# Kernel optimization log

Hardware: AMD Instinct MI355X
Metric: run time of the kernel (lower is better)

## Reference

```python
import jax, jax.numpy as jnp
import numpy as np


def _mlp(x, W1, b1, W2, b2):
    # x: (B, M, T); torch MLPLayer: transpose(1,2) -> Linear -> Linear -> LeakyReLU -> transpose back
    h = jnp.einsum('bmt,hm->bht', x, W1) + b1[None, :, None]   # (B, H, T)
    y = jnp.einsum('bht,oh->bot', h, W2) + b2[None, :, None]   # (B, M, T)
    return jax.nn.leaky_relu(y, negative_slope=0.01)


def _calc_attn(q, k, v):
    # q: (B, M, Tq), k: (B, M, Tk), v: (B, M, Tk)
    Tq = q.shape[-1]
    qk = jnp.einsum('bmq,bmk->bqk', q, k)                       # (B, Tq, Tk)
    eye = jnp.eye(Tq, dtype=qk.dtype)                           # broadcasts: (Tq,Tq) or (1,1)
    logits = jnp.exp(qk - qk * eye / jnp.sqrt(jnp.asarray(Tq, qk.dtype)))
    scores = jax.nn.softmax(logits, axis=-1)
    return jnp.einsum('bqk,bmk->bmq', scores, v)                # (B, M, Tq)


def setup_inputs() -> dict:
    key = jax.random.key(0)
    B, M, T, H = 16, 128, 2048, 512
    ks = jax.random.split(key, 14)
    s = 0.02
    inp = {
        'pattern': jax.random.normal(ks[0], (B, M, T), jnp.float32),
        'value': jax.random.normal(ks[1], (B, M, T), jnp.float32),
        'kernel_size': 33,
    }
    names = ['q', 'k', 'o']
    for i, n in enumerate(names):
        inp['W%s1' % n] = jax.random.normal(ks[2 + 4 * i], (H, M), jnp.float32) * s
        inp['b%s1' % n] = jax.random.normal(ks[3 + 4 * i], (H,), jnp.float32) * s
        inp['W%s2' % n] = jax.random.normal(ks[4 + 4 * i], (M, H), jnp.float32) * s
        inp['b%s2' % n] = jax.random.normal(ks[5 + 4 * i], (M,), jnp.float32) * s
    return inp


def reference(pattern, value, kernel_size, Wq1, bq1, Wq2, bq2, Wk1, bk1, Wk2, bk2, Wo1, bo1, Wo2, bo2):
    query = _mlp(pattern, Wq1, bq1, Wq2, bq2)
    key = _mlp(pattern, Wk1, bk1, Wk2, bk2)
    # full (internal) attention
    attn_in = _calc_attn(query, key, value)                     # (B, M, T)
    rep_in = _mlp(attn_in, Wo1, bo1, Wo2, bo2)
    # windowed (external) attention
    T = query.shape[-1]
    cu = (kernel_size - 1) // 2
    q_w = query[..., T - 1 - cu : T - cu]                       # (B, M, 1)
    k_w = key[..., kernel_size - cu - 1 : T - cu - 2]           # (B, M, T-k-1)
    v_w = value[..., kernel_size : T - 1]                       # (B, M, T-k-1)
    attn_ex = _calc_attn(q_w, k_w, v_w)                         # (B, M, 1)
    rep_ex = _mlp(attn_ex, Wo1, bo1, Wo2, bo2)
    return jnp.concatenate([rep_in, rep_ex], axis=-1)           # (B, M, T+1)
```

## Files before the change

### kernel.cpp

```cpp
#include <hip/hip_runtime.h>
#include <math.h>

#define B_    16
#define M_    128
#define T_    2048
#define H_    512
#define TOUT_ 2049

typedef unsigned short u16;
typedef unsigned int   u32;
typedef __bf16 bf16x8 __attribute__((ext_vector_type(8)));
typedef float  f32x16 __attribute__((ext_vector_type(16)));
typedef u32    u32x4  __attribute__((ext_vector_type(4)));
typedef u32    u32x2  __attribute__((ext_vector_type(2)));

#define A_OFF     0
#define C_OFF     49152
#define MEAN_OFF  49536
#define AQKBF_OFF 51584
#define AOBF_OFF  67968
#define QT_OFF    76160
#define KT_OFF    (76160 + 2097152)
#define VB_OFF    (76160 + 2 * 2097152)

static __device__ __forceinline__ u16 f2bf(float f) {
  u32 u = __float_as_uint(f);
  u = (u + 0x7FFFu + ((u >> 16) & 1u)) >> 16;
  return (u16)u;
}
static __device__ __forceinline__ u32 pk2(float lo, float hi) {
  return (u32)f2bf(lo) | ((u32)f2bf(hi) << 16);
}
static __device__ __forceinline__ bf16x8 ldfrag(const u16* p) {
  return __builtin_bit_cast(bf16x8, *(const u32x4*)p);
}

__global__ __launch_bounds__(128) void fuse_weights_all(
    const float* __restrict__ W1q, const float* __restrict__ b1q,
    const float* __restrict__ W2q, const float* __restrict__ b2q,
    const float* __restrict__ W1k, const float* __restrict__ b1k,
    const float* __restrict__ W2k, const float* __restrict__ b2k,
    const float* __restrict__ W1o, const float* __restrict__ b1o,
    const float* __restrict__ W2o, const float* __restrict__ b2o,
    float* __restrict__ A, float* __restrict__ c,
    u16* __restrict__ Aqk_bf, u16* __restrict__ Ao_bf) {
  __shared__ float w2row[H_];
  int which = blockIdx.x >> 7;
  int o = blockIdx.x & 127;
  const float* W1 = which == 0 ? W1q : which == 1 ? W1k : W1o;
  const float* b1 = which == 0 ? b1q : which == 1 ? b1k : b1o;
  const float* W2 = which == 0 ? W2q : which == 1 ? W2k : W2o;
  const float* b2 = which == 0 ? b2q : which == 1 ? b2k : b2o;
  int m = threadIdx.x;
  for (int h = m; h < H_; h += 128) w2row[h] = W2[o * H_ + h];
  __syncthreads();
  float acc = 0.f;
  for (int h = 0; h < H_; ++h) acc = fmaf(w2row[h], W1[h * M_ + m], acc);
  A[which * 16384 + o * M_ + m] = acc;
  u16 ab = f2bf(acc);
  if (which == 0)      Aqk_bf[o * 128 + m] = ab;
  else if (which == 1) Aqk_bf[(128 + o) * 128 + m] = ab;
  else                 Ao_bf[o * 128 + m] = ab;
  if (m == 0) {
    float cc = b2[o];
    for (int h = 0; h < H_; ++h) cc = fmaf(w2row[h], b1[h], cc);
    c[which * 128 + o] = cc;
  }
}

#define XSTR 136

__global__ __launch_bounds__(256) void mlp_qk_fused(
    const float* __restrict__ pattern, const u16* __restrict__ Aqk_bf,
    const float* __restrict__ cqk, u16* __restrict__ qT, u16* __restrict__ kT) {
  __shared__ alignas(16) u16 xs[64 * XSTR];
  int b = blockIdx.y;
  int t0 = blockIdx.x * 64;
  int tid = threadIdx.x;
  int lane = tid & 63;
  int wv = tid >> 6;
  int l31 = lane & 31;
  int lh8 = (lane >> 5) * 8;

  bf16x8 afr[2][8];
#pragma unroll
  for (int i = 0; i < 2; ++i) {
    const u16* ap = Aqk_bf + ((2 * wv + i) * 32 + l31) * 128 + lh8;
#pragma unroll
    for (int s = 0; s < 8; ++s) afr[i][s] = ldfrag(ap + 16 * s);
  }

  {
    int mp = tid & 63;
    int tc = tid >> 6;
    const float* r0 = pattern + ((size_t)(b * M_ + 2 * mp)) * T_ + t0 + tc * 16;
    const float* r1 = r0 + T_;
    u32* xw = (u32*)xs;
#pragma unroll
    for (int j = 0; j < 4; ++j) {
      float4 a = *(const float4*)(r0 + 4 * j);
      float4 bb = *(const float4*)(r1 + 4 * j);
      int tt = tc * 16 + 4 * j;
      xw[(tt + 0) * 68 + mp] = pk2(a.x, bb.x);
      xw[(tt + 1) * 68 + mp] = pk2(a.y, bb.y);
      xw[(tt + 2) * 68 + mp] = pk2(a.z, bb.z);
      xw[(tt + 3) * 68 + mp] = pk2(a.w, bb.w);
    }
  }
  __syncthreads();

#pragma unroll
  for (int tt = 0; tt < 2; ++tt) {
    bf16x8 bfr[8];
    const u16* bp = &xs[(tt * 32 + l31) * XSTR + lh8];
#pragma unroll
    for (int s = 0; s < 8; ++s) bfr[s] = ldfrag(bp + 16 * s);
#pragma unroll
    for (int i = 0; i < 2; ++i) {
      f32x16 acc;
#pragma unroll
      for (int r = 0; r < 16; ++r) acc[r] = 0.f;
#pragma unroll
      for (int s = 0; s < 8; ++s)
        acc = __builtin_amdgcn_mfma_f32_32x32x16_bf16(afr[i][s], bfr[s], acc, 0, 0, 0);
      int ot = 2 * wv + i;
      u16* dst = (ot < 4) ? qT : kT;
      int ob = (ot & 3) * 32;
      size_t trow = ((size_t)(b * T_ + t0 + tt * 32 + l31)) * 128;
#pragma unroll
      for (int g = 0; g < 4; ++g) {
        int o0 = 8 * g + 4 * (lane >> 5);
        float v0 = acc[4 * g + 0] + cqk[ot * 32 + o0 + 0];
        float v1 = acc[4 * g + 1] + cqk[ot * 32 + o0 + 1];
        float v2 = acc[4 * g + 2] + cqk[ot * 32 + o0 + 2];
        float v3 = acc[4 * g + 3] + cqk[ot * 32 + o0 + 3];
        v0 = v0 > 0.f ? v0 : 0.01f * v0;
        v1 = v1 > 0.f ? v1 : 0.01f * v1;
        v2 = v2 > 0.f ? v2 : 0.01f * v2;
        v3 = v3 > 0.f ? v3 : 0.01f * v3;
        u32x2 w = {pk2(v0, v1), pk2(v2, v3)};
        *(u32x2*)(dst + trow + ob + o0) = w;
      }
    }
  }
}

__global__ __launch_bounds__(256) void vcast_mean(
    const float* __restrict__ v, u16* __restrict__ vb, float* __restrict__ meanv) {
  __shared__ float red[256];
  int bm = blockIdx.x;
  int tid = threadIdx.x;
  const float* row = v + (size_t)bm * T_;
  int i0 = tid * 8;
  float4 a = *(const float4*)(row + i0);
  float4 bq = *(const float4*)(row + i0 + 4);
  u32x4 o = {pk2(a.x, a.y), pk2(a.z, a.w), pk2(bq.x, bq.y), pk2(bq.z, bq.w)};
  *(u32x4*)&vb[(size_t)bm * T_ + i0] = o;
  float vals[8] = {a.x, a.y, a.z, a.w, bq.x, bq.y, bq.z, bq.w};
  float s = 0.f;
#pragma unroll
  for (int j = 0; j < 8; ++j) {
    int idx = i0 + j;
    if (idx >= 33 && idx < T_ - 1) s += vals[j];
  }
  red[tid] = s;
  __syncthreads();
  for (int st = 128; st > 0; st >>= 1) {
    if (tid < st) red[tid] += red[tid + st];
    __syncthreads();
  }
  if (tid == 0) meanv[bm] = red[0] * (1.f / 2014.f);
}

#define TQ 64
#define TK 64
#define QSTR 136
#define VSTR 72

__global__ __launch_bounds__(256, 2) void attn_mfma_kernel(
    const u16* __restrict__ qT, const u16* __restrict__ kT,
    const u16* __restrict__ vB, const u16* __restrict__ Ao_bf,
    const float* __restrict__ co, float* __restrict__ out) {
  __shared__ alignas(16) u16 qs[TQ * QSTR];
  __shared__ alignas(16) u16 ks[TK * QSTR];
  __shared__ alignas(16) u16 vs[M_ * VSTR];
  __shared__ alignas(16) u16 wsm[TQ * VSTR];
  __shared__ float dls[2][TQ];

  int b = blockIdx.y;
  int q0 = blockIdx.x * TQ;
  int tid = threadIdx.x;
  int lane = tid & 63;
  int wv = tid >> 6;
  int l31 = lane & 31;
  int lh8 = (lane >> 5) * 8;

  {
    const u16* gq = qT + ((size_t)(b * T_ + q0)) * 128;
    for (int it = 0; it < 4; ++it) {
      int r = it * 16 + (tid >> 4);
      int cm = (tid & 15) * 8;
      *(u32x4*)&qs[r * QSTR + cm] = *(const u32x4*)&gq[r * 128 + cm];
    }
  }
  bf16x8 aofr[8];
  {
    const u16* ap = Ao_bf + (wv * 32 + l31) * 128 + lh8;
#pragma unroll
    for (int s = 0; s < 8; ++s) aofr[s] = ldfrag(ap + 16 * s);
  }
  __syncthreads();

  int qw = (wv >> 1) * 32;
  int kw = (wv & 1) * 32;
  bf16x8 afrag[8];
  {
    const u16* qrow = &qs[(qw + l31) * QSTR + lh8];
#pragma unroll
    for (int s = 0; s < 8; ++s) afrag[s] = ldfrag(qrow + s * 16);
  }

  int qt = wv & 1;
  int mb = (wv >> 1) * 2;

  f32x16 pacc[2];
  float dreg[16];
#pragma unroll
  for (int i = 0; i < 16; ++i) { pacc[0][i] = 0.f; pacc[1][i] = 0.f; dreg[i] = 0.f; }

  for (int kt = 0; kt < T_ / TK; ++kt) {
    int k0 = kt * TK;
    __syncthreads();
    {
      const u16* gk = kT + ((size_t)(b * T_ + k0)) * 128;
      for (int it = 0; it < 4; ++it) {
        int r = it * 16 + (tid >> 4);
        int cm = (tid & 15) * 8;
        *(u32x4*)&ks[r * QSTR + cm] = *(const u32x4*)&gk[r * 128 + cm];
      }
      const u16* gv = vB + (size_t)b * M_ * T_ + k0;
      for (int it = 0; it < 4; ++it) {
        int m = it * 32 + (tid >> 3);
        int ck = (tid & 7) * 8;
        *(u32x4*)&vs[m * VSTR + ck] = *(const u32x4*)&gv[(size_t)m * T_ + ck];
      }
    }
    __syncthreads();

    f32x16 sacc;
#pragma unroll
    for (int i = 0; i < 16; ++i) sacc[i] = 0.f;
    {
      const u16* krow = &ks[(kw + l31) * QSTR + lh8];
#pragma unroll
      for (int s = 0; s < 8; ++s) {
        bf16x8 bf = ldfrag(krow + s * 16);
        sacc = __builtin_amdgcn_mfma_f32_32x32x16_bf16(afrag[s], bf, sacc, 0, 0, 0);
      }
    }

    int kl = kw + l31;
    if (k0 == q0) {
#pragma unroll
      for (int r = 0; r < 16; ++r) {
        int qrow = qw + (r & 3) + 8 * (r >> 2) + 4 * (lane >> 5);
        if (qrow == kl) sacc[r] *= 0.97790291f;
      }
    }
#pragma unroll
    for (int r = 0; r < 16; ++r) {
      int qrow = qw + (r & 3) + 8 * (r >> 2) + 4 * (lane >> 5);
      float w = __expf(__expf(sacc[r]));
      u16 wb = f2bf(w);
      dreg[r] += __uint_as_float((u32)wb << 16);
      wsm[qrow * VSTR + kl] = wb;
    }
    __syncthreads();

#pragma unroll
    for (int s2 = 0; s2 < 4; ++s2) {
      bf16x8 wf = ldfrag(&wsm[(qt * 32 + l31) * VSTR + s2 * 16 + lh8]);
#pragma unroll
      for (int mi = 0; mi < 2; ++mi) {
        bf16x8 vf = ldfrag(&vs[((mb + mi) * 32 + l31) * VSTR + s2 * 16 + lh8]);
        pacc[mi] = __builtin_amdgcn_mfma_f32_32x32x16_bf16(vf, wf, pacc[mi], 0, 0, 0);
      }
    }
  }

#pragma unroll
  for (int r = 0; r < 16; ++r) {
    float d = dreg[r];
    for (int off = 1; off < 32; off <<= 1) d += __shfl_xor(d, off, 64);
    dreg[r] = d;
  }
  if (l31 == 0) {
#pragma unroll
    for (int r = 0; r < 16; ++r) {
      int qrow = qw + (r & 3) + 8 * (r >> 2) + 4 * (lane >> 5);
      dls[wv & 1][qrow] = dreg[r];
    }
  }
  __syncthreads();

  {
    int qcol = qt * 32 + l31;
    float rden = 1.f / (dls[0][qcol] + dls[1][qcol]);
#pragma unroll
    for (int mi = 0; mi < 2; ++mi) {
      int mbase = (mb + mi) * 32 + 4 * (lane >> 5);
#pragma unroll
      for (int g = 0; g < 4; ++g) {
        float v0 = pacc[mi][4 * g + 0] * rden;
        float v1 = pacc[mi][4 * g + 1] * rden;
        float v2 = pacc[mi][4 * g + 2] * rden;
        float v3 = pacc[mi][4 * g + 3] * rden;
        u32x2 w = {pk2(v0, v1), pk2(v2, v3)};
        *(u32x2*)&qs[qcol * QSTR + mbase + 8 * g] = w;
      }
    }
  }
  __syncthreads();

#pragma unroll
  for (int qt2 = 0; qt2 < 2; ++qt2) {
    bf16x8 pfr[8];
    const u16* pp = &qs[(qt2 * 32 + l31) * QSTR + lh8];
#pragma unroll
    for (int s = 0; s < 8; ++s) pfr[s] = ldfrag(pp + 16 * s);
    f32x16 oacc;
#pragma unroll
    for (int r = 0; r < 16; ++r) oacc[r] = 0.f;
#pragma unroll
    for (int s = 0; s < 8; ++s)
      oacc = __builtin_amdgcn_mfma_f32_32x32x16_bf16(aofr[s], pfr[s], oacc, 0, 0, 0);
#pragma unroll
    for (int r = 0; r < 16; ++r) {
      int orow = wv * 32 + (r & 3) + 8 * (r >> 2) + 4 * (lane >> 5);
      float v = oacc[r] + co[orow];
      v = v > 0.f ? v : 0.01f * v;
      out[((size_t)(b * M_ + orow)) * TOUT_ + q0 + qt2 * 32 + l31] = v;
    }
  }
}

__global__ __launch_bounds__(128) void rep_ex_kernel(
    const float* __restrict__ meanv, const float* __restrict__ A,
    const float* __restrict__ c, float* __restrict__ out) {
  __shared__ float xv[128];
  int b = blockIdx.x;
  int o = threadIdx.x;
  xv[o] = meanv[b * 128 + o];
  __syncthreads();
  float acc = c[o];
  for (int m = 0; m < 128; ++m) acc = fmaf(A[o * M_ + m], xv[m], acc);
  acc = acc > 0.f ? acc : 0.01f * acc;
  out[(b * M_ + o) * TOUT_ + 2048] = acc;
}

extern "C" void kernel_launch(void* const* d_in, const int* in_sizes, int n_in,
                              void* d_out, int out_size, void* d_ws, size_t ws_size,
                              hipStream_t stream) {
  (void)in_sizes; (void)n_in; (void)out_size; (void)ws_size;
  const float* pattern = (const float*)d_in[0];
  const float* value   = (const float*)d_in[1];
  const float* Wq1 = (const float*)d_in[3];
  const float* bq1 = (const float*)d_in[4];
  const float* Wq2 = (const float*)d_in[5];
  const float* bq2 = (const float*)d_in[6];
  const float* Wk1 = (const float*)d_in[7];
  const float* bk1 = (const float*)d_in[8];
  const float* Wk2 = (const float*)d_in[9];
  const float* bk2 = (const float*)d_in[10];
  const float* Wo1 = (const float*)d_in[11];
  const float* bo1 = (const float*)d_in[12];
  const float* Wo2 = (const float*)d_in[13];
  const float* bo2 = (const float*)d_in[14];

  float* ws     = (float*)d_ws;
  float* A      = ws + A_OFF;
  float* c      = ws + C_OFF;
  float* meanv  = ws + MEAN_OFF;
  u16*   Aqk_bf = (u16*)(ws + AQKBF_OFF);
  u16*   Ao_bf  = (u16*)(ws + AOBF_OFF);
  u16*   qT     = (u16*)(ws + QT_OFF);
  u16*   kT     = (u16*)(ws + KT_OFF);
  u16*   vB     = (u16*)(ws + VB_OFF);
  float* out    = (float*)d_out;

  fuse_weights_all<<<384, 128, 0, stream>>>(
      Wq1, bq1, Wq2, bq2, Wk1, bk1, Wk2, bk2, Wo1, bo1, Wo2, bo2,
      A, c, Aqk_bf, Ao_bf);

  mlp_qk_fused<<<dim3(T_ / 64, B_), 256, 0, stream>>>(pattern, Aqk_bf, c, qT, kT);
  vcast_mean<<<B_ * M_, 256, 0, stream>>>(value, vB, meanv);

  attn_mfma_kernel<<<dim3(T_ / TQ, B_), 256, 0, stream>>>(
      qT, kT, vB, Ao_bf, c + 256, out);

  rep_ex_kernel<<<B_, 128, 0, stream>>>(meanv, A + 32768, c + 256, out);
}
```

Baseline: 207.8 us.

## Merge prep kernels, prefetch K/V into registers, shrink attention LDS for occupancy

Folds the MLP q/k projection and the value cast/mean into one launch, and moves the windowed rep_ex computation into the tail of the attention kernel. This removes two kernel launches. In the attention loop, the next K/V tile is now loaded into registers while the current tile is computed. Shared memory is shrunk by aliasing the q, weight and denominator buffers, and launch bounds are raised to 3 blocks per CU, which adds register pressure from the prefetch buffers.

```diff
diff --git a/kernel.cpp b/kernel.cpp
--- a/kernel.cpp
+++ b/kernel.cpp
@@ -70,13 +70,43 @@
 
 #define XSTR 136
 
-__global__ __launch_bounds__(256) void mlp_qk_fused(
+__global__ __launch_bounds__(256) void prep_kernel(
     const float* __restrict__ pattern, const u16* __restrict__ Aqk_bf,
-    const float* __restrict__ cqk, u16* __restrict__ qT, u16* __restrict__ kT) {
-  __shared__ alignas(16) u16 xs[64 * XSTR];
-  int b = blockIdx.y;
-  int t0 = blockIdx.x * 64;
+    const float* __restrict__ cqk, u16* __restrict__ qT, u16* __restrict__ kT,
+    const float* __restrict__ value, u16* __restrict__ vb,
+    float* __restrict__ meanv) {
+  __shared__ alignas(16) u16 sxs[64 * XSTR];
+  int bx = blockIdx.x;
   int tid = threadIdx.x;
+
+  if (bx >= 512) {
+    int bm = bx - 512;
+    float* red = (float*)sxs;
+    const float* row = value + (size_t)bm * T_;
+    int i0 = tid * 8;
+    float4 a = *(const float4*)(row + i0);
+    float4 bq = *(const float4*)(row + i0 + 4);
+    u32x4 o = {pk2(a.x, a.y), pk2(a.z, a.w), pk2(bq.x, bq.y), pk2(bq.z, bq.w)};
+    *(u32x4*)&vb[(size_t)bm * T_ + i0] = o;
+    float vals[8] = {a.x, a.y, a.z, a.w, bq.x, bq.y, bq.z, bq.w};
+    float s = 0.f;
+#pragma unroll
+    for (int j = 0; j < 8; ++j) {
+      int idx = i0 + j;
+      if (idx >= 33 && idx < T_ - 1) s += vals[j];
+    }
+    red[tid] = s;
+    __syncthreads();
+    for (int st = 128; st > 0; st >>= 1) {
+      if (tid < st) red[tid] += red[tid + st];
+      __syncthreads();
+    }
+    if (tid == 0) meanv[bm] = red[0] * (1.f / 2014.f);
+    return;
+  }
+
+  int b = bx >> 5;
+  int t0 = (bx & 31) * 64;
   int lane = tid & 63;
   int wv = tid >> 6;
   int l31 = lane & 31;
@@ -95,7 +125,7 @@
     int tc = tid >> 6;
     const float* r0 = pattern + ((size_t)(b * M_ + 2 * mp)) * T_ + t0 + tc * 16;
     const float* r1 = r0 + T_;
-    u32* xw = (u32*)xs;
+    u32* xw = (u32*)sxs;
 #pragma unroll
     for (int j = 0; j < 4; ++j) {
       float4 a = *(const float4*)(r0 + 4 * j);
@@ -112,7 +142,7 @@
 #pragma unroll
   for (int tt = 0; tt < 2; ++tt) {
     bf16x8 bfr[8];
-    const u16* bp = &xs[(tt * 32 + l31) * XSTR + lh8];
+    const u16* bp = &sxs[(tt * 32 + l31) * XSTR + lh8];
 #pragma unroll
     for (int s = 0; s < 8; ++s) bfr[s] = ldfrag(bp + 16 * s);
 #pragma unroll
@@ -145,50 +175,21 @@
   }
 }
 
-__global__ __launch_bounds__(256) void vcast_mean(
-    const float* __restrict__ v, u16* __restrict__ vb, float* __restrict__ meanv) {
-  __shared__ float red[256];
-  int bm = blockIdx.x;
-  int tid = threadIdx.x;
-  const float* row = v + (size_t)bm * T_;
-  int i0 = tid * 8;
-  float4 a = *(const float4*)(row + i0);
-  float4 bq = *(const float4*)(row + i0 + 4);
-  u32x4 o = {pk2(a.x, a.y), pk2(a.z, a.w), pk2(bq.x, bq.y), pk2(bq.z, bq.w)};
-  *(u32x4*)&vb[(size_t)bm * T_ + i0] = o;
-  float vals[8] = {a.x, a.y, a.z, a.w, bq.x, bq.y, bq.z, bq.w};
-  float s = 0.f;
-#pragma unroll
-  for (int j = 0; j < 8; ++j) {
-    int idx = i0 + j;
-    if (idx >= 33 && idx < T_ - 1) s += vals[j];
-  }
-  red[tid] = s;
-  __syncthreads();
-  for (int st = 128; st > 0; st >>= 1) {
-    if (tid < st) red[tid] += red[tid + st];
-    __syncthreads();
-  }
-  if (tid == 0) meanv[bm] = red[0] * (1.f / 2014.f);
-}
-
-#define TQ 64
-#define TK 64
 #define QSTR 136
 #define VSTR 72
 
-__global__ __launch_bounds__(256, 2) void attn_mfma_kernel(
+__global__ __launch_bounds__(256, 3) void attn_mfma_kernel(
     const u16* __restrict__ qT, const u16* __restrict__ kT,
     const u16* __restrict__ vB, const u16* __restrict__ Ao_bf,
-    const float* __restrict__ co, float* __restrict__ out) {
-  __shared__ alignas(16) u16 qs[TQ * QSTR];
-  __shared__ alignas(16) u16 ks[TK * QSTR];
-  __shared__ alignas(16) u16 vs[M_ * VSTR];
-  __shared__ alignas(16) u16 wsm[TQ * VSTR];
-  __shared__ float dls[2][TQ];
+    const float* __restrict__ co, const float* __restrict__ Aofp,
+    const float* __restrict__ meanv, float* __restrict__ out) {
+  __shared__ alignas(16) u16 smem[26624];
+  u16* ks  = smem;
+  u16* vs  = smem + 8704;
+  u16* qsw = smem + 17920;
 
   int b = blockIdx.y;
-  int q0 = blockIdx.x * TQ;
+  int q0 = blockIdx.x * 64;
   int tid = threadIdx.x;
   int lane = tid & 63;
   int wv = tid >> 6;
@@ -196,18 +197,13 @@
   int lh8 = (lane >> 5) * 8;
 
   {
-    const u16* gq = qT + ((size_t)(b * T_ + q0)) * 128;
+    const u16* gq = qT + (size_t)(b * T_ + q0) * 128;
+#pragma unroll
     for (int it = 0; it < 4; ++it) {
       int r = it * 16 + (tid >> 4);
       int cm = (tid & 15) * 8;
-      *(u32x4*)&qs[r * QSTR + cm] = *(const u32x4*)&gq[r * 128 + cm];
-    }
-  }
-  bf16x8 aofr[8];
-  {
-    const u16* ap = Ao_bf + (wv * 32 + l31) * 128 + lh8;
-#pragma unroll
-    for (int s = 0; s < 8; ++s) aofr[s] = ldfrag(ap + 16 * s);
+      *(u32x4*)&qsw[r * QSTR + cm] = *(const u32x4*)&gq[r * 128 + cm];
+    }
   }
   __syncthreads();
 
@@ -215,7 +211,7 @@
   int kw = (wv & 1) * 32;
   bf16x8 afrag[8];
   {
-    const u16* qrow = &qs[(qw + l31) * QSTR + lh8];
+    const u16* qrow = &qsw[(qw + l31) * QSTR + lh8];
 #pragma unroll
     for (int s = 0; s < 8; ++s) afrag[s] = ldfrag(qrow + s * 16);
   }
@@ -228,24 +224,35 @@
 #pragma unroll
   for (int i = 0; i < 16; ++i) { pacc[0][i] = 0.f; pacc[1][i] = 0.f; dreg[i] = 0.f; }
 
-  for (int kt = 0; kt < T_ / TK; ++kt) {
-    int k0 = kt * TK;
+  const u16* gkb = kT + (size_t)b * T_ * 128;
+  const u16* gvb = vB + (size_t)b * M_ * T_;
+  int kr = tid >> 4, kc = (tid & 15) * 8;
+  int vr = tid >> 3, vc = (tid & 7) * 8;
+  u32x4 kreg[4], vreg[4];
+#pragma unroll
+  for (int it = 0; it < 4; ++it) {
+    kreg[it] = *(const u32x4*)&gkb[(size_t)(it * 16 + kr) * 128 + kc];
+    vreg[it] = *(const u32x4*)&gvb[(size_t)(it * 32 + vr) * T_ + vc];
+  }
+
+  for (int kt = 0; kt < T_ / 64; ++kt) {
+    int k0 = kt * 64;
     __syncthreads();
+#pragma unroll
+    for (int it = 0; it < 4; ++it) {
+      *(u32x4*)&ks[(it * 16 + kr) * QSTR + kc] = kreg[it];
+      *(u32x4*)&vs[(it * 32 + vr) * VSTR + vc] = vreg[it];
+    }
+    __syncthreads();
+
     {
-      const u16* gk = kT + ((size_t)(b * T_ + k0)) * 128;
+      int kn = (kt < T_ / 64 - 1) ? k0 + 64 : k0;
+#pragma unroll
       for (int it = 0; it < 4; ++it) {
-        int r = it * 16 + (tid >> 4);
-        int cm = (tid & 15) * 8;
-        *(u32x4*)&ks[r * QSTR + cm] = *(const u32x4*)&gk[r * 128 + cm];
-      }
-      const u16* gv = vB + (size_t)b * M_ * T_ + k0;
-      for (int it = 0; it < 4; ++it) {
-        int m = it * 32 + (tid >> 3);
-        int ck = (tid & 7) * 8;
-        *(u32x4*)&vs[m * VSTR + ck] = *(const u32x4*)&gv[(size_t)m * T_ + ck];
-      }
-    }
-    __syncthreads();
+        kreg[it] = *(const u32x4*)&gkb[(size_t)(kn + it * 16 + kr) * 128 + kc];
+        vreg[it] = *(const u32x4*)&gvb[(size_t)(it * 32 + vr) * T_ + kn + vc];
+      }
+    }
 
     f32x16 sacc;
 #pragma unroll
@@ -273,13 +280,13 @@
       float w = __expf(__expf(sacc[r]));
       u16 wb = f2bf(w);
       dreg[r] += __uint_as_float((u32)wb << 16);
-      wsm[qrow * VSTR + kl] = wb;
+      qsw[qrow * VSTR + kl] = wb;
     }
     __syncthreads();
 
 #pragma unroll
     for (int s2 = 0; s2 < 4; ++s2) {
-      bf16x8 wf = ldfrag(&wsm[(qt * 32 + l31) * VSTR + s2 * 16 + lh8]);
+      bf16x8 wf = ldfrag(&qsw[(qt * 32 + l31) * VSTR + s2 * 16 + lh8]);
 #pragma unroll
       for (int mi = 0; mi < 2; ++mi) {
         bf16x8 vf = ldfrag(&vs[((mb + mi) * 32 + l31) * VSTR + s2 * 16 + lh8]);
@@ -287,7 +294,9 @@
       }
     }
   }
-
+  __syncthreads();
+
+  float* dls = (float*)vs;
 #pragma unroll
   for (int r = 0; r < 16; ++r) {
     float d = dreg[r];
@@ -298,14 +307,14 @@
 #pragma unroll
     for (int r = 0; r < 16; ++r) {
       int qrow = qw + (r & 3) + 8 * (r >> 2) + 4 * (lane >> 5);
-      dls[wv & 1][qrow] = dreg[r];
+      dls[(wv & 1) * 64 + qrow] = dreg[r];
     }
   }
   __syncthreads();
 
   {
     int qcol = qt * 32 + l31;
-    float rden = 1.f / (dls[0][qcol] + dls[1][qcol]);
+    float rden = 1.f / (dls[qcol] + dls[64 + qcol]);
 #pragma unroll
     for (int mi = 0; mi < 2; ++mi) {
       int mbase = (mb + mi) * 32 + 4 * (lane >> 5);
@@ -316,16 +325,22 @@
         float v2 = pacc[mi][4 * g + 2] * rden;
         float v3 = pacc[mi][4 * g + 3] * rden;
         u32x2 w = {pk2(v0, v1), pk2(v2, v3)};
-        *(u32x2*)&qs[qcol * QSTR + mbase + 8 * g] = w;
-      }
-    }
-  }
-  __syncthreads();
-
+        *(u32x2*)&qsw[qcol * QSTR + mbase + 8 * g] = w;
+      }
+    }
+  }
+  __syncthreads();
+
+  bf16x8 aofr[8];
+  {
+    const u16* ap = Ao_bf + (wv * 32 + l31) * 128 + lh8;
+#pragma unroll
+    for (int s = 0; s < 8; ++s) aofr[s] = ldfrag(ap + 16 * s);
+  }
 #pragma unroll
   for (int qt2 = 0; qt2 < 2; ++qt2) {
     bf16x8 pfr[8];
-    const u16* pp = &qs[(qt2 * 32 + l31) * QSTR + lh8];
+    const u16* pp = &qsw[(qt2 * 32 + l31) * QSTR + lh8];
 #pragma unroll
     for (int s = 0; s < 8; ++s) pfr[s] = ldfrag(pp + 16 * s);
     f32x16 oacc;
@@ -342,20 +357,14 @@
       out[((size_t)(b * M_ + orow)) * TOUT_ + q0 + qt2 * 32 + l31] = v;
     }
   }
-}
-
-__global__ __launch_bounds__(128) void rep_ex_kernel(
-    const float* __restrict__ meanv, const float* __restrict__ A,
-    const float* __restrict__ c, float* __restrict__ out) {
-  __shared__ float xv[128];
-  int b = blockIdx.x;
-  int o = threadIdx.x;
-  xv[o] = meanv[b * 128 + o];
-  __syncthreads();
-  float acc = c[o];
-  for (int m = 0; m < 128; ++m) acc = fmaf(A[o * M_ + m], xv[m], acc);
-  acc = acc > 0.f ? acc : 0.01f * acc;
-  out[(b * M_ + o) * TOUT_ + 2048] = acc;
+
+  if (q0 == 0 && tid < 128) {
+    float acc = co[tid];
+    const float* mv = meanv + b * 128;
+    for (int m = 0; m < 128; ++m) acc = fmaf(Aofp[tid * 128 + m], mv[m], acc);
+    acc = acc > 0.f ? acc : 0.01f * acc;
+    out[((size_t)(b * M_ + tid)) * TOUT_ + 2048] = acc;
+  }
 }
 
 extern "C" void kernel_launch(void* const* d_in, const int* in_sizes, int n_in,
@@ -392,11 +401,9 @@
       Wq1, bq1, Wq2, bq2, Wk1, bk1, Wk2, bk2, Wo1, bo1, Wo2, bo2,
       A, c, Aqk_bf, Ao_bf);
 
-  mlp_qk_fused<<<dim3(T_ / 64, B_), 256, 0, stream>>>(pattern, Aqk_bf, c, qT, kT);
-  vcast_mean<<<B_ * M_, 256, 0, stream>>>(value, vB, meanv);
-
-  attn_mfma_kernel<<<dim3(T_ / TQ, B_), 256, 0, stream>>>(
-      qT, kT, vB, Ao_bf, c + 256, out);
-
-  rep_ex_kernel<<<B_, 128, 0, stream>>>(meanv, A + 32768, c + 256, out);
-}
+  prep_kernel<<<512 + B_ * M_, 256, 0, stream>>>(
+      pattern, Aqk_bf, c, qT, kT, value, vB, meanv);
+
+  attn_mfma_kernel<<<dim3(T_ / 64, B_), 256, 0, stream>>>(
+      qT, kT, vB, Ao_bf, c + 256, A + 32768, meanv, out);
+}
```

Result: faster. 202.7 us (-2.5%).
